# Kernel optimization log

Hardware: AMD Instinct MI355X
Metric: run time of the kernel (lower is better)

The kernel has to match this reference:

```python
import jax, jax.numpy as jnp
import numpy as np

D = 2048
N_HEAD = 16
D_HEAD = D // N_HEAD
EXP = 4
EPS = 1e-6


def setup_inputs() -> dict:
    key = jax.random.key(0)
    ks = jax.random.split(key, 8)
    b, s = 2, 2048
    scale = 0.02
    return {
        "x": jax.random.normal(ks[0], (b, s, D), dtype=jnp.float32),
        "w_qkv": jax.random.normal(ks[1], (D, 3 * D), dtype=jnp.float32) * scale,
        "w_o": jax.random.normal(ks[2], (D, D), dtype=jnp.float32) * scale,
        "w_up": jax.random.normal(ks[3], (D, EXP * D), dtype=jnp.float32) * scale,
        "w_gate": jax.random.normal(ks[4], (D, EXP * D), dtype=jnp.float32) * scale,
        "w_down": jax.random.normal(ks[5], (EXP * D, D), dtype=jnp.float32) * scale,
        "scale1": jnp.ones((D,), dtype=jnp.float32),
        "scale2": jnp.ones((D,), dtype=jnp.float32),
    }


def _rmsnorm(x, scale):
    rms = jnp.sqrt(jnp.mean(x * x, axis=-1, keepdims=True) + EPS)
    return x / rms * scale


def _attention(x, w_qkv, w_o):
    b, s, d = x.shape
    qkv = x @ w_qkv  # [b, s, 3d]
    q, k, v = jnp.split(qkv, 3, axis=-1)
    # [b, h, s, dh]
    q = q.reshape(b, s, N_HEAD, D_HEAD).transpose(0, 2, 1, 3)
    k = k.reshape(b, s, N_HEAD, D_HEAD).transpose(0, 2, 1, 3)
    v = v.reshape(b, s, N_HEAD, D_HEAD).transpose(0, 2, 1, 3)
    scores = jnp.einsum("bhqd,bhkd->bhqk", q, k) / np.sqrt(D_HEAD).astype(np.float32)
    causal = jnp.tril(jnp.ones((s, s), dtype=bool))
    scores = jnp.where(causal, scores, -jnp.inf)
    attn = jax.nn.softmax(scores, axis=-1)
    out = jnp.einsum("bhqk,bhkd->bhqd", attn, v)
    out = out.transpose(0, 2, 1, 3).reshape(b, s, d)
    return out @ w_o


def _mlp(x, w_up, w_gate, w_down):
    return (x @ w_up * jax.nn.silu(x @ w_gate)) @ w_down


def reference(x, w_qkv, w_o, w_up, w_gate, w_down, scale1, scale2):
    x = x + _attention(_rmsnorm(x, scale1), w_qkv, w_o)
    x = x + _mlp(_rmsnorm(x, scale2), w_up, w_gate, w_down)
    return x
```

## Files before the change

### kernel.cpp

```cpp
#include <hip/hip_runtime.h>

typedef unsigned short u16;
typedef __bf16 bfrag8 __attribute__((ext_vector_type(8)));
typedef float f32x4 __attribute__((ext_vector_type(4)));

#define MFMA16(a, b, c) __builtin_amdgcn_mfma_f32_16x16x32_bf16((a), (b), (c), 0, 0, 0)

static __device__ __forceinline__ u16 bf_bits(float f) {
  unsigned int u = __builtin_bit_cast(unsigned int, f);
  unsigned int r = (u + 0x7fffu + ((u >> 16) & 1u)) >> 16;
  return (u16)r;
}
static __device__ __forceinline__ float f_from_bits(u16 u) {
  unsigned int w = ((unsigned int)u) << 16;
  return __builtin_bit_cast(float, w);
}
static __device__ __forceinline__ void gload16(const void* g, void* l) {
  __builtin_amdgcn_global_load_lds(
      (const __attribute__((address_space(1))) void*)g,
      (__attribute__((address_space(3))) void*)l, 16, 0, 0);
}

__global__ __launch_bounds__(256) void k_transpose_bf16(const float* __restrict__ src,
                                                        u16* __restrict__ dst,
                                                        int K, int N) {
  __shared__ float tile[32][33];
  const int n0 = blockIdx.x * 32;
  const int k0 = blockIdx.y * 32;
  const int t = threadIdx.x;
  const int lr = t >> 5;
  const int lc = t & 31;
#pragma unroll
  for (int i = 0; i < 4; ++i)
    tile[lr + i * 8][lc] = src[(size_t)(k0 + lr + i * 8) * N + n0 + lc];
  __syncthreads();
#pragma unroll
  for (int i = 0; i < 4; ++i)
    dst[(size_t)(n0 + lr + i * 8) * K + k0 + lc] = bf_bits(tile[lc][lr + i * 8]);
}

__global__ __launch_bounds__(256) void k_transpose_v(const u16* __restrict__ qkv,
                                                     u16* __restrict__ vtg) {
  __shared__ u16 tile[32][33];
  const int bh = blockIdx.z, b = bh >> 4, hh = bh & 15;
  const int s0 = blockIdx.x * 32, d0 = blockIdx.y * 32;
  const int t = threadIdx.x;
  const int lr = t >> 5, lc = t & 31;
#pragma unroll
  for (int i = 0; i < 4; ++i)
    tile[lr + i * 8][lc] =
        qkv[(size_t)(b * 2048 + s0 + lr + i * 8) * 6144 + 4096 + hh * 128 + d0 + lc];
  __syncthreads();
#pragma unroll
  for (int i = 0; i < 4; ++i)
    vtg[(size_t)bh * 128 * 2048 + (size_t)(d0 + lr + i * 8) * 2048 + s0 + lc] =
        tile[lc][lr + i * 8];
}

__global__ __launch_bounds__(256) void k_rmsnorm(const float* __restrict__ x,
                                                 const float* __restrict__ sc,
                                                 u16* __restrict__ o) {
  const int row = blockIdx.x;
  const int t = threadIdx.x;
  const float4* x4 = (const float4*)(x + (size_t)row * 2048);
  float4 a = x4[t];
  float4 b = x4[t + 256];
  float ss = a.x * a.x + a.y * a.y + a.z * a.z + a.w * a.w +
             b.x * b.x + b.y * b.y + b.z * b.z + b.w * b.w;
#pragma unroll
  for (int off = 32; off > 0; off >>= 1) ss += __shfl_down(ss, off);
  __shared__ float red[4];
  if ((t & 63) == 0) red[t >> 6] = ss;
  __syncthreads();
  const float inv = rsqrtf((red[0] + red[1] + red[2] + red[3]) * (1.0f / 2048.0f) + 1e-6f);
  const float4* s4 = (const float4*)sc;
  float4 sa = s4[t], sb = s4[t + 256];
  ushort4 pa, pb;
  pa.x = bf_bits(a.x * inv * sa.x); pa.y = bf_bits(a.y * inv * sa.y);
  pa.z = bf_bits(a.z * inv * sa.z); pa.w = bf_bits(a.w * inv * sa.w);
  pb.x = bf_bits(b.x * inv * sb.x); pb.y = bf_bits(b.y * inv * sb.y);
  pb.z = bf_bits(b.z * inv * sb.z); pb.w = bf_bits(b.w * inv * sb.w);
  *(ushort4*)(o + (size_t)row * 2048 + t * 4) = pa;
  *(ushort4*)(o + (size_t)row * 2048 + (t + 256) * 4) = pb;
}

#define LDA(SB, H, MF, KH)                                                       \
  (*(const bfrag8*)(smC + (SB) * 65536 + (H) * 16384 +                           \
                    (wm * 64 + (MF) * 16 + l15) * 128 + (((KH) * 64 + lhi16) ^ swz)))
#define LDB(SB, NF, KH)                                                          \
  (*(const bfrag8*)(smC + (SB) * 65536 + 32768 +                                 \
                    (wn * 64 + (NF) * 16 + l15) * 128 + (((KH) * 64 + lhi16) ^ swz)))
#define STAGE_A(SB, H, KT)                                                       \
  {                                                                              \
    const u16* s_ = Asrc + (size_t)(H) * (64 * K) + (size_t)(KT) * 64;           \
    char* d_ = smC + (SB) * 65536 + (H) * 16384 + wchunk;                        \
    gload16(s_, d_);                                                             \
    gload16(s_ + 8 * K, d_ + 1024);                                              \
  }
#define STAGE_B(SB, C, KT)                                                       \
  {                                                                              \
    const u16* s_ = Bsrc + (size_t)(C) * (128 * K) + (size_t)(KT) * 64;          \
    char* d_ = smC + (SB) * 65536 + 32768 + (C) * 16384 + wchunk;                \
    gload16(s_, d_);                                                             \
    gload16(s_ + 8 * K, d_ + 1024);                                              \
  }
#define MM(H, I, J, AF, BF) acc[(H) * 4 + (I)][J] = MFMA16(AF, BF, acc[(H) * 4 + (I)][J])
#define PHASE(SB, H, KH, STAGE_STMT, TAIL_VM)                                    \
  {                                                                              \
    bfrag8 a0_ = LDA(SB, H, 0, KH), a1_ = LDA(SB, H, 1, KH),                     \
           a2_ = LDA(SB, H, 2, KH), a3_ = LDA(SB, H, 3, KH);                     \
    bfrag8 b0_ = LDB(SB, 0, KH), b1_ = LDB(SB, 1, KH),                           \
           b2_ = LDB(SB, 2, KH), b3_ = LDB(SB, 3, KH);                           \
    STAGE_STMT;                                                                  \
    __builtin_amdgcn_s_barrier();                                                \
    __builtin_amdgcn_s_setprio(1);                                               \
    MM(H, 0, 0, a0_, b0_); MM(H, 0, 1, a0_, b1_);                                \
    MM(H, 0, 2, a0_, b2_); MM(H, 0, 3, a0_, b3_);                                \
    MM(H, 1, 0, a1_, b0_); MM(H, 1, 1, a1_, b1_);                                \
    MM(H, 1, 2, a1_, b2_); MM(H, 1, 3, a1_, b3_);                                \
    MM(H, 2, 0, a2_, b0_); MM(H, 2, 1, a2_, b1_);                                \
    MM(H, 2, 2, a2_, b2_); MM(H, 2, 3, a2_, b3_);                                \
    MM(H, 3, 0, a3_, b0_); MM(H, 3, 1, a3_, b1_);                                \
    MM(H, 3, 2, a3_, b2_); MM(H, 3, 3, a3_, b3_);                                \
    __builtin_amdgcn_s_setprio(0);                                               \
    TAIL_VM;                                                                     \
    __builtin_amdgcn_s_barrier();                                                \
  }
#define VM2 asm volatile("s_waitcnt vmcnt(2)" ::: "memory")
#define NOPVM (void)0

template <int EPI, int K>
__global__ __launch_bounds__(512, 2) void k_gemm8(const u16* __restrict__ A,
                                                  const u16* __restrict__ Bt,
                                                  int M, int N,
                                                  float* __restrict__ outF,
                                                  u16* __restrict__ outB,
                                                  const float* __restrict__ resid,
                                                  const u16* __restrict__ gate) {
  __shared__ u16 sm[2 * 32768];
  char* smC = (char*)sm;
  const int t = threadIdx.x;
  const int nbx = gridDim.x;
  const int nwg = nbx * gridDim.y;
  int f = blockIdx.x + nbx * blockIdx.y;
  f = (f & 7) * (nwg >> 3) + (f >> 3);
  const int m0 = (f / nbx) * 256;
  const int n0 = (f % nbx) * 256;

  const int wid = t >> 6, lane = t & 63;
  const int wm = wid >> 2, wn = wid & 3;
  const int l15 = lane & 15, lhi = lane >> 4;
  const int lhi16 = lhi * 16;
  const int swz = (l15 & 7) << 4;

  f32x4 acc[8][4];
#pragma unroll
  for (int i = 0; i < 8; ++i)
#pragma unroll
    for (int j = 0; j < 4; ++j) acc[i][j] = (f32x4){0.f, 0.f, 0.f, 0.f};

  const int sr = lane >> 3;
  const int csw = (((lane & 7) * 16) ^ (sr << 4)) >> 1;
  const u16* Asrc =
      A + (size_t)(m0 + (wid >> 2) * 128 + (wid & 3) * 16 + sr) * K + csw;
  const u16* Bsrc = Bt + (size_t)(n0 + wid * 16 + sr) * K + csw;
  const unsigned wchunk = (unsigned)wid * 2048 + (unsigned)lane * 16;

  const int NT = K >> 6;

  STAGE_A(0, 0, 0);
  STAGE_A(0, 1, 0);
  STAGE_B(0, 0, 0);
  STAGE_B(0, 1, 0);
  STAGE_A(1, 0, 1);
  VM2;
  __builtin_amdgcn_s_barrier();

  for (int it = 0; it < (NT >> 1); ++it) {
    const int kt1 = 2 * it + 1;
    const int kt2 = (2 * it + 2 < NT) ? 2 * it + 2 : NT - 1;
    const int kt3 = (2 * it + 3 < NT) ? 2 * it + 3 : NT - 1;
    PHASE(0, 0, 0, STAGE_A(1, 1, kt1), NOPVM);
    PHASE(0, 1, 0, STAGE_B(1, 0, kt1), NOPVM);
    PHASE(0, 0, 1, STAGE_B(1, 1, kt1), NOPVM);
    PHASE(0, 1, 1, STAGE_A(0, 0, kt2), VM2);
    PHASE(1, 0, 0, STAGE_B(0, 0, kt2), NOPVM);
    PHASE(1, 1, 0, STAGE_B(0, 1, kt2), NOPVM);
    PHASE(1, 0, 1, STAGE_A(0, 1, kt2), NOPVM);
    PHASE(1, 1, 1, STAGE_A(1, 0, kt3), VM2);
  }

#pragma unroll
  for (int mf = 0; mf < 8; ++mf) {
#pragma unroll
    for (int nf = 0; nf < 4; ++nf) {
      const int mr = m0 + wm * 128 + mf * 16 + lhi * 4;
      const int nc = n0 + wn * 64 + nf * 16 + l15;
#pragma unroll
      for (int r = 0; r < 4; ++r) {
        const size_t idx = (size_t)(mr + r) * N + nc;
        const float v = acc[mf][nf][r];
        if (EPI == 0) {
          outB[idx] = bf_bits(v);
        } else if (EPI == 1) {
          outF[idx] = resid[idx] + v;
        } else {
          float g = f_from_bits(gate[idx]);
          float s = g / (1.f + __expf(-g));
          outB[idx] = bf_bits(v * s);
        }
      }
    }
  }
}

__global__ __launch_bounds__(512) void k_attn(const u16* __restrict__ qkv,
                                              const u16* __restrict__ vtg,
                                              u16* __restrict__ out) {
  const int S = 2048, LD = 6144;
  const float scale = 0.0883883476483184405f;
  const int bh = blockIdx.y;
  const int b = bh >> 4, hh = bh & 15;
  const int qt = (b == 0) ? (15 - (int)blockIdx.x) : (int)blockIdx.x;
  const int t = threadIdx.x;
  const int wave = t >> 6, lane = t & 63;
  const int l15 = lane & 15, lhi = lane >> 4;
  const int lhi16 = lhi * 16;
  const int swz = (l15 & 7) << 4;

  __shared__ u16 Kt[64 * 128];
  __shared__ u16 Vt[128 * 64];
  __shared__ u16 Pl[8][16][72];
  char* KtC = (char*)Kt;
  char* VtC = (char*)Vt;

  const int qrow = qt * 128 + wave * 16 + l15;
  const size_t qoff = (size_t)(b * S + qrow) * LD + hh * 128 + lhi * 8;
  bfrag8 qf[4];
#pragma unroll
  for (int ks = 0; ks < 4; ++ks) qf[ks] = *(const bfrag8*)(qkv + qoff + ks * 32);

  f32x4 oacc[8];
#pragma unroll
  for (int j = 0; j < 8; ++j) oacc[j] = (f32x4){0.f, 0.f, 0.f, 0.f};
  float m_i[4], l_i[4];
#pragma unroll
  for (int r = 0; r < 4; ++r) { m_i[r] = -INFINITY; l_i[r] = 0.f; }

  const int q_my = qt * 128 + wave * 16 + lhi * 4;
  const int q_wave_last = qt * 128 + wave * 16 + 15;

  const int keyA = t >> 4, keyB = 32 + (t >> 4);
  const int oK = (t & 15) * 16;
  const int dA = t >> 3, dB = 64 + (t >> 3);
  const int oV = (t & 7) * 16;
  const u16* kbase = qkv + (size_t)(b * S) * LD + 2048 + hh * 128;
  const u16* vbase = vtg + (size_t)bh * 128 * S;
  const u16* ksrcA = kbase + (size_t)keyA * LD + ((oK ^ ((keyA & 7) << 4)) >> 1);
  const u16* ksrcB = kbase + (size_t)keyB * LD + ((oK ^ ((keyB & 7) << 4)) >> 1);
  const u16* vsrcA = vbase + (size_t)dA * S + ((oV ^ ((dA & 7) << 4)) >> 1);
  const u16* vsrcB = vbase + (size_t)dB * S + ((oV ^ ((dB & 7) << 4)) >> 1);
  const unsigned int ldso0 = wave * 1024 + lane * 16;
  const unsigned int ldso1 = 8192 + wave * 1024 + lane * 16;
  const size_t kstep = (size_t)64 * LD;

  const int kt_max = 2 * qt + 1;
  for (int kt = 0; kt <= kt_max; ++kt) {
    __syncthreads();
    gload16(ksrcA + (size_t)kt * kstep, KtC + ldso0);
    gload16(ksrcB + (size_t)kt * kstep, KtC + ldso1);
    gload16(vsrcA + kt * 64, VtC + ldso0);
    gload16(vsrcB + kt * 64, VtC + ldso1);
    __syncthreads();

    if (kt * 64 <= q_wave_last) {
      f32x4 sfr[4];
#pragma unroll
      for (int j = 0; j < 4; ++j) {
        sfr[j] = (f32x4){0.f, 0.f, 0.f, 0.f};
        const int krow = j * 16 + l15;
#pragma unroll
        for (int ks = 0; ks < 4; ++ks) {
          bfrag8 kf = *(const bfrag8*)(KtC + krow * 256 + ((ks * 64 + lhi16) ^ swz));
          sfr[j] = MFMA16(qf[ks], kf, sfr[j]);
        }
      }
      float sv[4][4], rmax[4];
#pragma unroll
      for (int r = 0; r < 4; ++r) rmax[r] = -INFINITY;
#pragma unroll
      for (int j = 0; j < 4; ++j) {
        const int key = kt * 64 + j * 16 + l15;
#pragma unroll
        for (int r = 0; r < 4; ++r) {
          float v = sfr[j][r] * scale;
          v = (key <= q_my + r) ? v : -INFINITY;
          sv[j][r] = v;
          rmax[r] = fmaxf(rmax[r], v);
        }
      }
#pragma unroll
      for (int r = 0; r < 4; ++r) {
        float v = rmax[r];
        v = fmaxf(v, __shfl_xor(v, 1));
        v = fmaxf(v, __shfl_xor(v, 2));
        v = fmaxf(v, __shfl_xor(v, 4));
        v = fmaxf(v, __shfl_xor(v, 8));
        rmax[r] = v;
      }
      float alpha[4], rsum[4];
#pragma unroll
      for (int r = 0; r < 4; ++r) {
        float mn = fmaxf(m_i[r], rmax[r]);
        alpha[r] = __expf(m_i[r] - mn);
        m_i[r] = mn;
        rsum[r] = 0.f;
      }
#pragma unroll
      for (int j = 0; j < 4; ++j) {
#pragma unroll
        for (int r = 0; r < 4; ++r) {
          float p = __expf(sv[j][r] - m_i[r]);
          rsum[r] += p;
          Pl[wave][lhi * 4 + r][j * 16 + l15] = bf_bits(p);
        }
      }
#pragma unroll
      for (int r = 0; r < 4; ++r) {
        float v = rsum[r];
        v += __shfl_xor(v, 1); v += __shfl_xor(v, 2);
        v += __shfl_xor(v, 4); v += __shfl_xor(v, 8);
        l_i[r] = l_i[r] * alpha[r] + v;
      }
#pragma unroll
      for (int j = 0; j < 8; ++j)
#pragma unroll
        for (int r = 0; r < 4; ++r) oacc[j][r] *= alpha[r];

#pragma unroll
      for (int ks2 = 0; ks2 < 2; ++ks2) {
        bfrag8 pf = *(const bfrag8*)&Pl[wave][l15][ks2 * 32 + lhi * 8];
#pragma unroll
        for (int j = 0; j < 8; ++j) {
          const int d = j * 16 + l15;
          bfrag8 vf = *(const bfrag8*)(VtC + d * 128 + ((ks2 * 64 + lhi16) ^ swz));
          oacc[j] = MFMA16(pf, vf, oacc[j]);
        }
      }
    }
  }

#pragma unroll
  for (int r = 0; r < 4; ++r) {
    const float inv = 1.f / l_i[r];
    const size_t tok = (size_t)b * S + qt * 128 + wave * 16 + lhi * 4 + r;
#pragma unroll
    for (int j = 0; j < 8; ++j)
      out[tok * 2048 + hh * 128 + j * 16 + l15] = bf_bits(oacc[j][r] * inv);
  }
}

extern "C" void kernel_launch(void* const* d_in, const int* in_sizes, int n_in,
                              void* d_out, int out_size, void* d_ws, size_t ws_size,
                              hipStream_t stream) {
  (void)in_sizes; (void)n_in; (void)out_size; (void)ws_size;
  const float* x      = (const float*)d_in[0];
  const float* w_qkv  = (const float*)d_in[1];
  const float* w_o    = (const float*)d_in[2];
  const float* w_up   = (const float*)d_in[3];
  const float* w_gate = (const float*)d_in[4];
  const float* w_down = (const float*)d_in[5];
  const float* scale1 = (const float*)d_in[6];
  const float* scale2 = (const float*)d_in[7];
  float* out = (float*)d_out;

  u16* B       = (u16*)d_ws;
  u16* wqkvT   = B;
  u16* woT     = wqkvT  + (size_t)6144 * 2048;
  u16* wgateT  = woT    + (size_t)2048 * 2048;
  u16* wupT    = wgateT + (size_t)8192 * 2048;
  u16* wdownT  = wupT   + (size_t)8192 * 2048;
  u16* xn      = wdownT + (size_t)2048 * 8192;
  u16* qkvb    = xn     + (size_t)4096 * 2048;
  u16* attnb   = qkvb   + (size_t)4096 * 6144;
  float* y1    = (float*)(attnb + (size_t)4096 * 2048);
  u16* vtg     = (u16*)y1;
  u16* gbuf    = qkvb;
  u16* hbuf    = wqkvT;

  dim3 blk(256);
  k_transpose_bf16<<<dim3(192, 64), blk, 0, stream>>>(w_qkv,  wqkvT,  2048, 6144);
  k_transpose_bf16<<<dim3(64, 64),  blk, 0, stream>>>(w_o,    woT,    2048, 2048);
  k_transpose_bf16<<<dim3(256, 64), blk, 0, stream>>>(w_gate, wgateT, 2048, 8192);
  k_transpose_bf16<<<dim3(256, 64), blk, 0, stream>>>(w_up,   wupT,   2048, 8192);
  k_transpose_bf16<<<dim3(64, 256), blk, 0, stream>>>(w_down, wdownT, 8192, 2048);

  k_rmsnorm<<<4096, blk, 0, stream>>>(x, scale1, xn);
  k_gemm8<0, 2048><<<dim3(24, 16), dim3(512), 0, stream>>>(xn, wqkvT, 4096, 6144, nullptr, qkvb, nullptr, nullptr);
  k_transpose_v<<<dim3(64, 4, 32), blk, 0, stream>>>(qkvb, vtg);
  k_attn<<<dim3(16, 32), dim3(512), 0, stream>>>(qkvb, vtg, attnb);
  k_gemm8<1, 2048><<<dim3(8, 16), dim3(512), 0, stream>>>(attnb, woT, 4096, 2048, y1, nullptr, x, nullptr);
  k_rmsnorm<<<4096, blk, 0, stream>>>(y1, scale2, xn);
  k_gemm8<0, 2048><<<dim3(32, 16), dim3(512), 0, stream>>>(xn, wgateT, 4096, 8192, nullptr, gbuf, nullptr, nullptr);
  k_gemm8<2, 2048><<<dim3(32, 16), dim3(512), 0, stream>>>(xn, wupT, 4096, 8192, nullptr, hbuf, nullptr, gbuf);
  k_gemm8<1, 8192><<<dim3(8, 16), dim3(512), 0, stream>>>(hbuf, wdownT, 4096, 2048, out, nullptr, y1, nullptr);
}
```

Measured before the change: 915.4 us.

## Software-pipeline LDS fragment reads with double-buffered registers in GEMM mainloop

Restructures the GEMM main loop so the LDS-to-register fragment reads for the next MFMA phase are issued while the current phase computes, using ping-pong register arrays for A and B fragments. Global-to-LDS staging is regrouped into pairs and waits become vmcnt(0) at two points per iteration, with a reordered barrier layout. It aims to hide LDS read latency behind MFMAs. In exchange it raises register pressure and shortens how far ahead global prefetch runs, which can expose global-load latency.

Result: no change. 916.4 us (+0.1%).

```diff
diff --git a/kernel.cpp b/kernel.cpp
--- a/kernel.cpp
+++ b/kernel.cpp
@@ -90,6 +90,12 @@
 #define LDB(SB, NF, KH)                                                          \
   (*(const bfrag8*)(smC + (SB) * 65536 + 32768 +                                 \
                     (wn * 64 + (NF) * 16 + l15) * 128 + (((KH) * 64 + lhi16) ^ swz)))
+#define RDA(PX, SB, H, KH)                                                       \
+  aF##PX[0] = LDA(SB, H, 0, KH); aF##PX[1] = LDA(SB, H, 1, KH);                  \
+  aF##PX[2] = LDA(SB, H, 2, KH); aF##PX[3] = LDA(SB, H, 3, KH);
+#define RDB(PX, SB, KH)                                                          \
+  bF##PX[0] = LDB(SB, 0, KH); bF##PX[1] = LDB(SB, 1, KH);                        \
+  bF##PX[2] = LDB(SB, 2, KH); bF##PX[3] = LDB(SB, 3, KH);
 #define STAGE_A(SB, H, KT)                                                       \
   {                                                                              \
     const u16* s_ = Asrc + (size_t)(H) * (64 * K) + (size_t)(KT) * 64;           \
@@ -104,30 +110,27 @@
     gload16(s_, d_);                                                             \
     gload16(s_ + 8 * K, d_ + 1024);                                              \
   }
-#define MM(H, I, J, AF, BF) acc[(H) * 4 + (I)][J] = MFMA16(AF, BF, acc[(H) * 4 + (I)][J])
-#define PHASE(SB, H, KH, STAGE_STMT, TAIL_VM)                                    \
-  {                                                                              \
-    bfrag8 a0_ = LDA(SB, H, 0, KH), a1_ = LDA(SB, H, 1, KH),                     \
-           a2_ = LDA(SB, H, 2, KH), a3_ = LDA(SB, H, 3, KH);                     \
-    bfrag8 b0_ = LDB(SB, 0, KH), b1_ = LDB(SB, 1, KH),                           \
-           b2_ = LDB(SB, 2, KH), b3_ = LDB(SB, 3, KH);                           \
-    STAGE_STMT;                                                                  \
-    __builtin_amdgcn_s_barrier();                                                \
-    __builtin_amdgcn_s_setprio(1);                                               \
-    MM(H, 0, 0, a0_, b0_); MM(H, 0, 1, a0_, b1_);                                \
-    MM(H, 0, 2, a0_, b2_); MM(H, 0, 3, a0_, b3_);                                \
-    MM(H, 1, 0, a1_, b0_); MM(H, 1, 1, a1_, b1_);                                \
-    MM(H, 1, 2, a1_, b2_); MM(H, 1, 3, a1_, b3_);                                \
-    MM(H, 2, 0, a2_, b0_); MM(H, 2, 1, a2_, b1_);                                \
-    MM(H, 2, 2, a2_, b2_); MM(H, 2, 3, a2_, b3_);                                \
-    MM(H, 3, 0, a3_, b0_); MM(H, 3, 1, a3_, b1_);                                \
-    MM(H, 3, 2, a3_, b2_); MM(H, 3, 3, a3_, b3_);                                \
-    __builtin_amdgcn_s_setprio(0);                                               \
-    TAIL_VM;                                                                     \
-    __builtin_amdgcn_s_barrier();                                                \
-  }
-#define VM2 asm volatile("s_waitcnt vmcnt(2)" ::: "memory")
-#define NOPVM (void)0
+#define MFMAS(H, PA, PB)                                                         \
+  acc[(H)*4+0][0] = MFMA16(aF##PA[0], bF##PB[0], acc[(H)*4+0][0]);               \
+  acc[(H)*4+0][1] = MFMA16(aF##PA[0], bF##PB[1], acc[(H)*4+0][1]);               \
+  acc[(H)*4+0][2] = MFMA16(aF##PA[0], bF##PB[2], acc[(H)*4+0][2]);               \
+  acc[(H)*4+0][3] = MFMA16(aF##PA[0], bF##PB[3], acc[(H)*4+0][3]);               \
+  acc[(H)*4+1][0] = MFMA16(aF##PA[1], bF##PB[0], acc[(H)*4+1][0]);               \
+  acc[(H)*4+1][1] = MFMA16(aF##PA[1], bF##PB[1], acc[(H)*4+1][1]);               \
+  acc[(H)*4+1][2] = MFMA16(aF##PA[1], bF##PB[2], acc[(H)*4+1][2]);               \
+  acc[(H)*4+1][3] = MFMA16(aF##PA[1], bF##PB[3], acc[(H)*4+1][3]);               \
+  acc[(H)*4+2][0] = MFMA16(aF##PA[2], bF##PB[0], acc[(H)*4+2][0]);               \
+  acc[(H)*4+2][1] = MFMA16(aF##PA[2], bF##PB[1], acc[(H)*4+2][1]);               \
+  acc[(H)*4+2][2] = MFMA16(aF##PA[2], bF##PB[2], acc[(H)*4+2][2]);               \
+  acc[(H)*4+2][3] = MFMA16(aF##PA[2], bF##PB[3], acc[(H)*4+2][3]);               \
+  acc[(H)*4+3][0] = MFMA16(aF##PA[3], bF##PB[0], acc[(H)*4+3][0]);               \
+  acc[(H)*4+3][1] = MFMA16(aF##PA[3], bF##PB[1], acc[(H)*4+3][1]);               \
+  acc[(H)*4+3][2] = MFMA16(aF##PA[3], bF##PB[2], acc[(H)*4+3][2]);               \
+  acc[(H)*4+3][3] = MFMA16(aF##PA[3], bF##PB[3], acc[(H)*4+3][3]);
+#define SBAR __builtin_amdgcn_s_barrier()
+#define PRIO1 __builtin_amdgcn_s_setprio(1)
+#define PRIO0 __builtin_amdgcn_s_setprio(0)
+#define VM0 asm volatile("s_waitcnt vmcnt(0)" ::: "memory")
 
 template <int EPI, int K>
 __global__ __launch_bounds__(512, 2) void k_gemm8(const u16* __restrict__ A,
@@ -166,28 +169,44 @@
   const u16* Bsrc = Bt + (size_t)(n0 + wid * 16 + sr) * K + csw;
   const unsigned wchunk = (unsigned)wid * 2048 + (unsigned)lane * 16;
 
+  bfrag8 aF0[4], aF1[4], bF0[4], bF1[4];
+
   const int NT = K >> 6;
 
   STAGE_A(0, 0, 0);
   STAGE_A(0, 1, 0);
   STAGE_B(0, 0, 0);
   STAGE_B(0, 1, 0);
-  STAGE_A(1, 0, 1);
-  VM2;
-  __builtin_amdgcn_s_barrier();
+  VM0;
+  SBAR;
+  RDA(0, 0, 0, 0);
+  RDB(0, 0, 0);
 
   for (int it = 0; it < (NT >> 1); ++it) {
     const int kt1 = 2 * it + 1;
     const int kt2 = (2 * it + 2 < NT) ? 2 * it + 2 : NT - 1;
-    const int kt3 = (2 * it + 3 < NT) ? 2 * it + 3 : NT - 1;
-    PHASE(0, 0, 0, STAGE_A(1, 1, kt1), NOPVM);
-    PHASE(0, 1, 0, STAGE_B(1, 0, kt1), NOPVM);
-    PHASE(0, 0, 1, STAGE_B(1, 1, kt1), NOPVM);
-    PHASE(0, 1, 1, STAGE_A(0, 0, kt2), VM2);
-    PHASE(1, 0, 0, STAGE_B(0, 0, kt2), NOPVM);
-    PHASE(1, 1, 0, STAGE_B(0, 1, kt2), NOPVM);
-    PHASE(1, 0, 1, STAGE_A(0, 1, kt2), NOPVM);
-    PHASE(1, 1, 1, STAGE_A(1, 0, kt3), VM2);
+    SBAR; PRIO1; MFMAS(0, 0, 0); PRIO0;
+    STAGE_A(1, 0, kt1); STAGE_A(1, 1, kt1);
+    RDA(1, 0, 1, 0);
+    SBAR; PRIO1; MFMAS(1, 1, 0); PRIO0;
+    STAGE_B(1, 0, kt1); STAGE_B(1, 1, kt1);
+    RDA(0, 0, 0, 1); RDB(1, 0, 1);
+    SBAR; PRIO1; MFMAS(0, 0, 1); PRIO0;
+    RDA(1, 0, 1, 1);
+    VM0;
+    SBAR; PRIO1; MFMAS(1, 1, 1); PRIO0;
+    RDA(0, 1, 0, 0); RDB(0, 1, 0);
+    SBAR; PRIO1; MFMAS(0, 0, 0); PRIO0;
+    STAGE_A(0, 0, kt2); STAGE_A(0, 1, kt2);
+    RDA(1, 1, 1, 0);
+    SBAR; PRIO1; MFMAS(1, 1, 0); PRIO0;
+    STAGE_B(0, 0, kt2); STAGE_B(0, 1, kt2);
+    RDA(0, 1, 0, 1); RDB(1, 1, 1);
+    SBAR; PRIO1; MFMAS(0, 0, 1); PRIO0;
+    RDA(1, 1, 1, 1);
+    VM0;
+    SBAR; PRIO1; MFMAS(1, 1, 1); PRIO0;
+    RDA(0, 0, 0, 0); RDB(0, 0, 0);
   }
 
 #pragma unroll
```
